# Performance work log

Measured on AMD Instinct MI355X. Metric: run time of the kernel, lower is better.

The kernel has to match this reference:

```python
import jax, jax.numpy as jnp
import numpy as np

B, N, C_IN = 32, 4096, 32
C_OUT = 64
K = 5            # poly_degree
P = 4            # pooling_size
NNZ = 65536      # N * avg_degree(16)


def setup_inputs() -> dict:
    key = jax.random.key(0)
    ks = jax.random.split(key, 6)
    x = jax.random.normal(ks[0], (B, N, C_IN), dtype=jnp.float32)
    # scale edge values so the Chebyshev recursion stays numerically bounded
    edge_val = jax.random.normal(ks[1], (NNZ,), dtype=jnp.float32) * 0.05
    weight = jax.random.normal(ks[2], (K * C_IN, C_OUT), dtype=jnp.float32) * 0.1
    bias = jax.random.normal(ks[3], (1, 1, C_OUT), dtype=jnp.float32) * 0.1
    edge_row = jax.random.randint(ks[4], (NNZ,), 0, N, dtype=jnp.int32)
    edge_col = jax.random.randint(ks[5], (NNZ,), 0, N, dtype=jnp.int32)
    return {"x": x, "edge_val": edge_val, "weight": weight, "bias": bias,
            "edge_row": edge_row, "edge_col": edge_col}


def reference(x, edge_val, weight, bias, edge_row, edge_col):
    b, n, c = x.shape
    out_f = weight.shape[1]
    k_deg = weight.shape[0] // c

    def spmm(v):  # sparse (COO) L @ v, v: [n, c*b]
        gathered = v[edge_col] * edge_val[:, None]          # [nnz, c*b]
        return jax.ops.segment_sum(gathered, edge_row, num_segments=n)

    # x0: [n, c*b]
    x0 = jnp.transpose(x, (1, 2, 0)).reshape(n, c * b)
    x_list = [x0]
    if k_deg > 1:
        x1 = spmm(x0)
        x_list.append(x1)
    for _ in range(2, k_deg):
        x2 = 2.0 * spmm(x1) - x0
        x_list.append(x2)
        x0, x1 = x1, x2

    xs = jnp.stack(x_list, axis=0)                          # [K, n, c, b] after reshape
    xs = xs.reshape(k_deg, n, c, b)
    xs = jnp.transpose(xs, (3, 1, 2, 0))                    # [b, n, c, K]
    xs = xs.reshape(b * n, c * k_deg)
    y = (xs @ weight).reshape(b, n, out_f)                  # dense GEMM

    y = jax.nn.relu(y + bias)                               # bias + ReLU

    if P > 1:  # max pool of size P over node dim
        y = y.reshape(b, n // P, P, out_f).max(axis=2)
    return y
```

## Files before the change

kernel.cpp:

```cpp
#include <hip/hip_runtime.h>

#define BATCH 32
#define NNODE 4096
#define CIN 32
#define COUT 64
#define KDEG 5
#define POOL 4
#define NNZ_E 65536
#define BC (BATCH * CIN)
#define TBF ((size_t)NNODE * BC)
#define CAP 64

typedef short s16x8 __attribute__((ext_vector_type(8)));
typedef float f32x4 __attribute__((ext_vector_type(4)));
typedef unsigned long long u64;

__device__ __forceinline__ unsigned short f2bf(float f) {
    union { float f; unsigned int u; } v; v.f = f;
    unsigned int u = v.u;
    u += 0x7fffu + ((u >> 16) & 1u);
    return (unsigned short)(u >> 16);
}
__device__ __forceinline__ float bf2f(unsigned short b) {
    union { float f; unsigned int u; } v; v.u = ((unsigned int)b) << 16;
    return v.f;
}
__device__ __forceinline__ u64 pack4(float a, float b, float c, float d) {
    return (u64)f2bf(a) | ((u64)f2bf(b) << 16) | ((u64)f2bf(c) << 32) | ((u64)f2bf(d) << 48);
}


__global__ void prep2_kernel(const float* __restrict__ x, unsigned short* __restrict__ t0,
                             const int* __restrict__ erow, const int* __restrict__ ecol,
                             const float* __restrict__ eval,
                             int* __restrict__ cnt, int2* __restrict__ es,
                             const float* __restrict__ W, unsigned short* __restrict__ WB) {
    int idx = blockIdx.x * 256 + threadIdx.x;
    int n   = idx >> 8;
    int rem = idx & 255;
    int b   = rem >> 3;
    int c4  = rem & 7;
    float4 v = ((const float4*)x)[(b * NNODE + n) * 8 + c4];
    ((u64*)t0)[idx] = pack4(v.x, v.y, v.z, v.w);

    if (idx < NNZ_E) {
        int r = erow[idx];
        int pos = atomicAdd(&cnt[r], 1);
        if (pos < CAP)
            es[(r << 6) + pos] = make_int2(ecol[idx], __float_as_int(eval[idx]));
    }

    if (idx < KDEG * COUT * CIN) {
        int c = idx & 31;
        int rest = idx >> 5;
        int o = rest & 63;
        int k = rest >> 6;
        WB[idx] = f2bf(W[(c * KDEG + k) * COUT + o]);
    }
}


__device__ __forceinline__ u64 spmm_row(
        const unsigned short* in, const unsigned short* sub,
        float scale, int has_sub, const int* cnt, const int2* es,
        int r, int sc, int ep) {
    const u64* in8 = (const u64*)in;
    int deg = cnt[r]; deg = deg > CAP ? CAP : deg;
    int beg = r << 6, end = beg + deg;

    float4 a0 = make_float4(0.f, 0.f, 0.f, 0.f);
    float4 a1 = a0, a2 = a0, a3 = a0;

    for (int base = beg + ep; base < end; base += 8) {
        float vv[4];
        u64   xx[4];
#pragma unroll
        for (int j = 0; j < 4; j++) {
            int idx = base + 2 * j;
            int src = idx < end ? idx : beg;
            int2 e = es[src];
            vv[j] = idx < end ? __int_as_float(e.y) : 0.f;
            xx[j] = in8[(size_t)e.x * 256 + sc];
        }
        a0.x += vv[0] * bf2f((unsigned short)xx[0]);
        a0.y += vv[0] * bf2f((unsigned short)(xx[0] >> 16));
        a0.z += vv[0] * bf2f((unsigned short)(xx[0] >> 32));
        a0.w += vv[0] * bf2f((unsigned short)(xx[0] >> 48));
        a1.x += vv[1] * bf2f((unsigned short)xx[1]);
        a1.y += vv[1] * bf2f((unsigned short)(xx[1] >> 16));
        a1.z += vv[1] * bf2f((unsigned short)(xx[1] >> 32));
        a1.w += vv[1] * bf2f((unsigned short)(xx[1] >> 48));
        a2.x += vv[2] * bf2f((unsigned short)xx[2]);
        a2.y += vv[2] * bf2f((unsigned short)(xx[2] >> 16));
        a2.z += vv[2] * bf2f((unsigned short)(xx[2] >> 32));
        a2.w += vv[2] * bf2f((unsigned short)(xx[2] >> 48));
        a3.x += vv[3] * bf2f((unsigned short)xx[3]);
        a3.y += vv[3] * bf2f((unsigned short)(xx[3] >> 16));
        a3.z += vv[3] * bf2f((unsigned short)(xx[3] >> 32));
        a3.w += vv[3] * bf2f((unsigned short)(xx[3] >> 48));
    }

    float4 acc;
    acc.x = (a0.x + a1.x) + (a2.x + a3.x);
    acc.y = (a0.y + a1.y) + (a2.y + a3.y);
    acc.z = (a0.z + a1.z) + (a2.z + a3.z);
    acc.w = (a0.w + a1.w) + (a2.w + a3.w);

    acc.x += __shfl_xor(acc.x, 32);
    acc.y += __shfl_xor(acc.y, 32);
    acc.z += __shfl_xor(acc.z, 32);
    acc.w += __shfl_xor(acc.w, 32);

    if (ep != 0) return 0;

    size_t oi = (size_t)r * 256 + sc;
    float r0, r1, r2, r3;
    if (has_sub) {
        u64 sv = __builtin_nontemporal_load((const u64*)sub + oi);
        r0 = scale * acc.x - bf2f((unsigned short)sv);
        r1 = scale * acc.y - bf2f((unsigned short)(sv >> 16));
        r2 = scale * acc.z - bf2f((unsigned short)(sv >> 32));
        r3 = scale * acc.w - bf2f((unsigned short)(sv >> 48));
    } else {
        r0 = acc.x; r1 = acc.y; r2 = acc.z; r3 = acc.w;
    }
    return pack4(r0, r1, r2, r3);
}


__global__ __launch_bounds__(256) void spmm_lvl_kernel(
        const unsigned short* __restrict__ in, const unsigned short* __restrict__ sub,
        unsigned short* __restrict__ out, float scale, int has_sub,
        const int* __restrict__ cnt, const int2* __restrict__ es) {
    int bx    = blockIdx.x;
    int slice = bx & 7;
    int rg    = bx >> 3;
    int wave  = threadIdx.x >> 6;
    int lane  = threadIdx.x & 63;
    int ep    = lane >> 5;
    int c     = lane & 31;
    int r     = rg * 4 + wave;
    int sc    = slice * 32 + c;

    u64 res = spmm_row(in, sub, scale, has_sub, cnt, es, r, sc, ep);
    if (ep == 0)
        ((u64*)out)[(size_t)r * 256 + sc] = res;
}


__global__ __launch_bounds__(256) void spmm4_gemm_kernel(
        const unsigned short* __restrict__ t3, const unsigned short* __restrict__ t2,
        const unsigned short* __restrict__ tbase, const int* __restrict__ cnt,
        const int2* __restrict__ es, const unsigned short* __restrict__ WB,
        const float* __restrict__ bias, float* __restrict__ out) {
    __shared__ u64 t4l[16][33];

    int tid  = threadIdx.x;
    int wv   = tid >> 6;
    int lane = tid & 63;
    int bid  = blockIdx.x;
    int s    = bid & 7;
    int n0   = (bid >> 3) << 4;

    int ep = lane >> 5;
    int c  = lane & 31;
    int sc = s * 32 + c;
#pragma unroll
    for (int i = 0; i < 4; i++) {
        int r = n0 + i * 4 + wv;
        u64 res = spmm_row(t3, t2, 2.0f, 1, cnt, es, r, sc, ep);
        if (ep == 0)
            t4l[i * 4 + wv][c] = res;
    }
    __syncthreads();

    int m = lane & 15;
    int q = lane >> 4;
    int b = s * 4 + wv;

    f32x4 acc[4] = {{0.f,0.f,0.f,0.f},{0.f,0.f,0.f,0.f},
                    {0.f,0.f,0.f,0.f},{0.f,0.f,0.f,0.f}};

    const unsigned short* abase = tbase + (size_t)(n0 + m) * BC + b * CIN + q * 8;
    const unsigned short* wbase = WB + m * 32 + q * 8;

#pragma unroll
    for (int k = 0; k < KDEG - 1; k++) {
        s16x8 a = *(const s16x8*)(abase + (size_t)k * TBF);
#pragma unroll
        for (int ot = 0; ot < 4; ot++) {
            s16x8 bf = *(const s16x8*)(wbase + ((k * 64) + ot * 16) * 32);
            acc[ot] = __builtin_amdgcn_mfma_f32_16x16x32_bf16(a, bf, acc[ot], 0, 0, 0);
        }
    }
    {
        union { u64 u[2]; s16x8 v; } cvt;
        cvt.u[0] = t4l[m][wv * 8 + q * 2];
        cvt.u[1] = t4l[m][wv * 8 + q * 2 + 1];
#pragma unroll
        for (int ot = 0; ot < 4; ot++) {
            s16x8 bf = *(const s16x8*)(wbase + ((4 * 64) + ot * 16) * 32);
            acc[ot] = __builtin_amdgcn_mfma_f32_16x16x32_bf16(cvt.v, bf, acc[ot], 0, 0, 0);
        }
    }

    size_t orow = ((size_t)b * (NNODE / POOL) + (n0 >> 2) + q) * COUT;
#pragma unroll
    for (int ot = 0; ot < 4; ot++) {
        float bi = bias[ot * 16 + m];
        float r0 = acc[ot][0] + bi; r0 = r0 > 0.f ? r0 : 0.f;
        float r1 = acc[ot][1] + bi; r1 = r1 > 0.f ? r1 : 0.f;
        float r2 = acc[ot][2] + bi; r2 = r2 > 0.f ? r2 : 0.f;
        float r3 = acc[ot][3] + bi; r3 = r3 > 0.f ? r3 : 0.f;
        float mx = r0 > r1 ? r0 : r1;
        mx = mx > r2 ? mx : r2;
        mx = mx > r3 ? mx : r3;
        out[orow + ot * 16 + m] = mx;
    }
}


extern "C" void kernel_launch(void* const* d_in, const int* in_sizes, int n_in,
                              void* d_out, int out_size, void* d_ws, size_t ws_size,
                              hipStream_t stream) {
    const float* x    = (const float*)d_in[0];
    const float* eval = (const float*)d_in[1];
    const float* W    = (const float*)d_in[2];
    const float* bias = (const float*)d_in[3];
    const int*   erow = (const int*)d_in[4];
    const int*   ecol = (const int*)d_in[5];
    float* out = (float*)d_out;

    char* base = (char*)d_ws;
    unsigned short* tb = (unsigned short*)base;
    unsigned short* t0 = tb;
    unsigned short* t1 = tb + 1 * TBF;
    unsigned short* t2 = tb + 2 * TBF;
    unsigned short* t3 = tb + 3 * TBF;

    size_t off = 5 * TBF * sizeof(unsigned short);
    int2* es = (int2*)(base + off);  off += (size_t)NNODE * CAP * sizeof(int2);
    int* cnt = (int*)(base + off);   off += (size_t)NNODE * sizeof(int);
    off += 32 * sizeof(int);
    off = (off + 63) & ~(size_t)63;
    unsigned short* WB = (unsigned short*)(base + off);

    hipMemsetAsync(cnt, 0, NNODE * sizeof(int), stream);

    prep2_kernel<<<TBF / 4 / 256, 256, 0, stream>>>(x, t0, erow, ecol, eval,
                                                    cnt, es, W, WB);

    spmm_lvl_kernel<<<NNODE * 2, 256, 0, stream>>>(t0, nullptr, t1, 1.0f, 0, cnt, es);
    spmm_lvl_kernel<<<NNODE * 2, 256, 0, stream>>>(t1, t0, t2, 2.0f, 1, cnt, es);
    spmm_lvl_kernel<<<NNODE * 2, 256, 0, stream>>>(t2, t1, t3, 2.0f, 1, cnt, es);

    spmm4_gemm_kernel<<<2048, 256, 0, stream>>>(t3, t2, tb, cnt, es, WB, bias, out);
}
```

Before: 190.4 us.

## Widen SpMM gathers to 16-byte loads and split fused GEMM across 16 waves

The SpMM row routine now has each lane load 8 bf16 values (16 bytes) per neighbor and splits edges four ways across 16-lane groups, reducing with two shuffles, instead of 4 values per lane with a two-way split. The fused SpMM+GEMM kernel moves from 256 to 1024 threads: each wave computes one row of the last SpMM level and then one 16-column output tile of the MFMA GEMM, instead of four rows and four tiles. The goal is fewer, wider memory transactions and more parallel waves, paid for with more shuffle reduction and larger blocks that may limit occupancy. Launch-bounds hints for occupancy are also added.

```diff
diff --git a/kernel.cpp b/kernel.cpp
--- a/kernel.cpp
+++ b/kernel.cpp
@@ -60,75 +60,69 @@
 }
 
 
-__device__ __forceinline__ u64 spmm_row(
+__device__ __forceinline__ s16x8 spmm_row4(
         const unsigned short* in, const unsigned short* sub,
         float scale, int has_sub, const int* cnt, const int2* es,
-        int r, int sc, int ep) {
-    const u64* in8 = (const u64*)in;
+        int r, int s, int lane) {
+    int ep  = lane >> 4;
+    int c16 = lane & 15;
+    const s16x8* in16 = (const s16x8*)in;
+
     int deg = cnt[r]; deg = deg > CAP ? CAP : deg;
     int beg = r << 6, end = beg + deg;
 
-    float4 a0 = make_float4(0.f, 0.f, 0.f, 0.f);
-    float4 a1 = a0, a2 = a0, a3 = a0;
-
-    for (int base = beg + ep; base < end; base += 8) {
+    float acc[8] = {0.f,0.f,0.f,0.f,0.f,0.f,0.f,0.f};
+
+    for (int base = beg + ep; base < end; base += 16) {
         float vv[4];
-        u64   xx[4];
+        s16x8 xx[4];
 #pragma unroll
         for (int j = 0; j < 4; j++) {
-            int idx = base + 2 * j;
+            int idx = base + 4 * j;
             int src = idx < end ? idx : beg;
             int2 e = es[src];
             vv[j] = idx < end ? __int_as_float(e.y) : 0.f;
-            xx[j] = in8[(size_t)e.x * 256 + sc];
+            xx[j] = in16[(size_t)e.x * 128 + s * 16 + c16];
         }
-        a0.x += vv[0] * bf2f((unsigned short)xx[0]);
-        a0.y += vv[0] * bf2f((unsigned short)(xx[0] >> 16));
-        a0.z += vv[0] * bf2f((unsigned short)(xx[0] >> 32));
-        a0.w += vv[0] * bf2f((unsigned short)(xx[0] >> 48));
-        a1.x += vv[1] * bf2f((unsigned short)xx[1]);
-        a1.y += vv[1] * bf2f((unsigned short)(xx[1] >> 16));
-        a1.z += vv[1] * bf2f((unsigned short)(xx[1] >> 32));
-        a1.w += vv[1] * bf2f((unsigned short)(xx[1] >> 48));
-        a2.x += vv[2] * bf2f((unsigned short)xx[2]);
-        a2.y += vv[2] * bf2f((unsigned short)(xx[2] >> 16));
-        a2.z += vv[2] * bf2f((unsigned short)(xx[2] >> 32));
-        a2.w += vv[2] * bf2f((unsigned short)(xx[2] >> 48));
-        a3.x += vv[3] * bf2f((unsigned short)xx[3]);
-        a3.y += vv[3] * bf2f((unsigned short)(xx[3] >> 16));
-        a3.z += vv[3] * bf2f((unsigned short)(xx[3] >> 32));
-        a3.w += vv[3] * bf2f((unsigned short)(xx[3] >> 48));
-    }
-
-    float4 acc;
-    acc.x = (a0.x + a1.x) + (a2.x + a3.x);
-    acc.y = (a0.y + a1.y) + (a2.y + a3.y);
-    acc.z = (a0.z + a1.z) + (a2.z + a3.z);
-    acc.w = (a0.w + a1.w) + (a2.w + a3.w);
-
-    acc.x += __shfl_xor(acc.x, 32);
-    acc.y += __shfl_xor(acc.y, 32);
-    acc.z += __shfl_xor(acc.z, 32);
-    acc.w += __shfl_xor(acc.w, 32);
-
-    if (ep != 0) return 0;
-
-    size_t oi = (size_t)r * 256 + sc;
-    float r0, r1, r2, r3;
-    if (has_sub) {
-        u64 sv = __builtin_nontemporal_load((const u64*)sub + oi);
-        r0 = scale * acc.x - bf2f((unsigned short)sv);
-        r1 = scale * acc.y - bf2f((unsigned short)(sv >> 16));
-        r2 = scale * acc.z - bf2f((unsigned short)(sv >> 32));
-        r3 = scale * acc.w - bf2f((unsigned short)(sv >> 48));
-    } else {
-        r0 = acc.x; r1 = acc.y; r2 = acc.z; r3 = acc.w;
-    }
-    return pack4(r0, r1, r2, r3);
-}
-
-
-__global__ __launch_bounds__(256) void spmm_lvl_kernel(
+#pragma unroll
+        for (int j = 0; j < 4; j++)
+#pragma unroll
+            for (int t = 0; t < 8; t++)
+                acc[t] += vv[j] * bf2f((unsigned short)xx[j][t]);
+    }
+
+#pragma unroll
+    for (int t = 0; t < 8; t++) {
+        acc[t] += __shfl_xor(acc[t], 16);
+        acc[t] += __shfl_xor(acc[t], 32);
+    }
+
+    union { u64 u[2]; s16x8 v; } res;
+    res.u[0] = 0; res.u[1] = 0;
+    if (ep == 0) {
+        size_t oi = (size_t)r * 128 + s * 16 + c16;
+        float rr[8];
+        if (has_sub) {
+            u64 sv0 = __builtin_nontemporal_load((const u64*)sub + 2 * oi);
+            u64 sv1 = __builtin_nontemporal_load((const u64*)sub + 2 * oi + 1);
+#pragma unroll
+            for (int t = 0; t < 4; t++)
+                rr[t] = scale * acc[t] - bf2f((unsigned short)(sv0 >> (16 * t)));
+#pragma unroll
+            for (int t = 0; t < 4; t++)
+                rr[4 + t] = scale * acc[4 + t] - bf2f((unsigned short)(sv1 >> (16 * t)));
+        } else {
+#pragma unroll
+            for (int t = 0; t < 8; t++) rr[t] = acc[t];
+        }
+        res.u[0] = pack4(rr[0], rr[1], rr[2], rr[3]);
+        res.u[1] = pack4(rr[4], rr[5], rr[6], rr[7]);
+    }
+    return res.v;
+}
+
+
+__global__ __launch_bounds__(256, 8) void spmm_lvl_kernel(
         const unsigned short* __restrict__ in, const unsigned short* __restrict__ sub,
         unsigned short* __restrict__ out, float scale, int has_sub,
         const int* __restrict__ cnt, const int2* __restrict__ es) {
@@ -137,86 +131,69 @@
     int rg    = bx >> 3;
     int wave  = threadIdx.x >> 6;
     int lane  = threadIdx.x & 63;
-    int ep    = lane >> 5;
-    int c     = lane & 31;
     int r     = rg * 4 + wave;
-    int sc    = slice * 32 + c;
-
-    u64 res = spmm_row(in, sub, scale, has_sub, cnt, es, r, sc, ep);
-    if (ep == 0)
-        ((u64*)out)[(size_t)r * 256 + sc] = res;
-}
-
-
-__global__ __launch_bounds__(256) void spmm4_gemm_kernel(
+
+    s16x8 res = spmm_row4(in, sub, scale, has_sub, cnt, es, r, slice, lane);
+    if (lane < 16)
+        ((s16x8*)out)[(size_t)r * 128 + slice * 16 + lane] = res;
+}
+
+
+__global__ __launch_bounds__(1024, 8) void spmm4_gemm_kernel(
         const unsigned short* __restrict__ t3, const unsigned short* __restrict__ t2,
         const unsigned short* __restrict__ tbase, const int* __restrict__ cnt,
         const int2* __restrict__ es, const unsigned short* __restrict__ WB,
         const float* __restrict__ bias, float* __restrict__ out) {
-    __shared__ u64 t4l[16][33];
+    __shared__ s16x8 t4l[16][19];
 
     int tid  = threadIdx.x;
-    int wv   = tid >> 6;
+    int w    = tid >> 6;
     int lane = tid & 63;
     int bid  = blockIdx.x;
     int s    = bid & 7;
     int n0   = (bid >> 3) << 4;
 
-    int ep = lane >> 5;
-    int c  = lane & 31;
-    int sc = s * 32 + c;
-#pragma unroll
-    for (int i = 0; i < 4; i++) {
-        int r = n0 + i * 4 + wv;
-        u64 res = spmm_row(t3, t2, 2.0f, 1, cnt, es, r, sc, ep);
-        if (ep == 0)
-            t4l[i * 4 + wv][c] = res;
+    {
+        int r = n0 + w;
+        s16x8 res = spmm_row4(t3, t2, 2.0f, 1, cnt, es, r, s, lane);
+        if (lane < 16)
+            t4l[w][lane] = res;
     }
     __syncthreads();
 
-    int m = lane & 15;
-    int q = lane >> 4;
-    int b = s * 4 + wv;
-
-    f32x4 acc[4] = {{0.f,0.f,0.f,0.f},{0.f,0.f,0.f,0.f},
-                    {0.f,0.f,0.f,0.f},{0.f,0.f,0.f,0.f}};
+    int m    = lane & 15;
+    int q    = lane >> 4;
+    int bsub = w & 3;
+    int ot   = w >> 2;
+    int b    = s * 4 + bsub;
+
+    f32x4 acc = {0.f, 0.f, 0.f, 0.f};
 
     const unsigned short* abase = tbase + (size_t)(n0 + m) * BC + b * CIN + q * 8;
-    const unsigned short* wbase = WB + m * 32 + q * 8;
+    const unsigned short* wbase = WB + m * 32 + q * 8 + (ot * 16) * 32;
 
 #pragma unroll
     for (int k = 0; k < KDEG - 1; k++) {
         s16x8 a = *(const s16x8*)(abase + (size_t)k * TBF);
-#pragma unroll
-        for (int ot = 0; ot < 4; ot++) {
-            s16x8 bf = *(const s16x8*)(wbase + ((k * 64) + ot * 16) * 32);
-            acc[ot] = __builtin_amdgcn_mfma_f32_16x16x32_bf16(a, bf, acc[ot], 0, 0, 0);
-        }
+        s16x8 bf = *(const s16x8*)(wbase + (k * 64) * 32);
+        acc = __builtin_amdgcn_mfma_f32_16x16x32_bf16(a, bf, acc, 0, 0, 0);
     }
     {
-        union { u64 u[2]; s16x8 v; } cvt;
-        cvt.u[0] = t4l[m][wv * 8 + q * 2];
-        cvt.u[1] = t4l[m][wv * 8 + q * 2 + 1];
-#pragma unroll
-        for (int ot = 0; ot < 4; ot++) {
-            s16x8 bf = *(const s16x8*)(wbase + ((4 * 64) + ot * 16) * 32);
-            acc[ot] = __builtin_amdgcn_mfma_f32_16x16x32_bf16(cvt.v, bf, acc[ot], 0, 0, 0);
-        }
+        s16x8 a = t4l[m][bsub * 4 + q];
+        s16x8 bf = *(const s16x8*)(wbase + (4 * 64) * 32);
+        acc = __builtin_amdgcn_mfma_f32_16x16x32_bf16(a, bf, acc, 0, 0, 0);
     }
 
     size_t orow = ((size_t)b * (NNODE / POOL) + (n0 >> 2) + q) * COUT;
-#pragma unroll
-    for (int ot = 0; ot < 4; ot++) {
-        float bi = bias[ot * 16 + m];
-        float r0 = acc[ot][0] + bi; r0 = r0 > 0.f ? r0 : 0.f;
-        float r1 = acc[ot][1] + bi; r1 = r1 > 0.f ? r1 : 0.f;
-        float r2 = acc[ot][2] + bi; r2 = r2 > 0.f ? r2 : 0.f;
-        float r3 = acc[ot][3] + bi; r3 = r3 > 0.f ? r3 : 0.f;
-        float mx = r0 > r1 ? r0 : r1;
-        mx = mx > r2 ? mx : r2;
-        mx = mx > r3 ? mx : r3;
-        out[orow + ot * 16 + m] = mx;
-    }
+    float bi = bias[ot * 16 + m];
+    float r0 = acc[0] + bi; r0 = r0 > 0.f ? r0 : 0.f;
+    float r1 = acc[1] + bi; r1 = r1 > 0.f ? r1 : 0.f;
+    float r2 = acc[2] + bi; r2 = r2 > 0.f ? r2 : 0.f;
+    float r3 = acc[3] + bi; r3 = r3 > 0.f ? r3 : 0.f;
+    float mx = r0 > r1 ? r0 : r1;
+    mx = mx > r2 ? mx : r2;
+    mx = mx > r3 ? mx : r3;
+    out[orow + ot * 16 + m] = mx;
 }
 
 
@@ -254,5 +231,5 @@
     spmm_lvl_kernel<<<NNODE * 2, 256, 0, stream>>>(t1, t0, t2, 2.0f, 1, cnt, es);
     spmm_lvl_kernel<<<NNODE * 2, 256, 0, stream>>>(t2, t1, t3, 2.0f, 1, cnt, es);
 
-    spmm4_gemm_kernel<<<2048, 256, 0, stream>>>(t3, t2, tb, cnt, es, WB, bias, out);
-}
+    spmm4_gemm_kernel<<<2048, 1024, 0, stream>>>(t3, t2, tb, cnt, es, WB, bias, out);
+}
```

Result: faster. 176.1 us (-7.5%).
